# Optimization experiments

Measured on AMD Instinct MI355X. Metric: run time of the kernel, lower is better.

## Reference

```python
import jax, jax.numpy as jnp
import numpy as np

B, N, E, H = 8, 1024, 768, 8
D = E // H  # 96

def setup_inputs() -> dict:
    key = jax.random.key(0)
    ks = jax.random.split(key, 5)
    s = 0.02
    return {
        "x": jax.random.normal(ks[0], (B, N, E), dtype=jnp.float32),
        "Wqkv": jax.random.normal(ks[1], (E, 3 * E), dtype=jnp.float32) * s,
        "bqkv": jax.random.normal(ks[2], (3 * E,), dtype=jnp.float32) * s,
        "Wproj": jax.random.normal(ks[3], (E, E), dtype=jnp.float32) * s,
        "bproj": jax.random.normal(ks[4], (E,), dtype=jnp.float32) * s,
    }

def reference(x, Wqkv, bqkv, Wproj, bproj):
    # qkv: [B,N,3E] -> split as (h d qkv), qkv fastest-varying -> [B,N,H,D,3]
    qkv = (x @ Wqkv + bqkv).reshape(B, N, H, D, 3)
    q = jnp.transpose(qkv[..., 0], (0, 2, 1, 3))  # [B,H,N,D]
    k = jnp.transpose(qkv[..., 1], (0, 2, 1, 3))
    v = jnp.transpose(qkv[..., 2], (0, 2, 1, 3))
    scale = E ** (-0.5)  # note: emb_size, not head_dim (faithful to source)
    scores = jnp.einsum('bhqd,bhkd->bhqk', q, k) * scale
    attn = jax.nn.softmax(scores, axis=-1)
    out = jnp.einsum('bhqk,bhkd->bhqd', attn, v)  # [B,H,N,D]
    out = jnp.transpose(out, (0, 2, 1, 3)).reshape(B, N, E)
    return out @ Wproj + bproj
```

## Files before the change

kernel.cpp:

```cpp
#include <hip/hip_runtime.h>

typedef unsigned short u16;
typedef __attribute__((ext_vector_type(8))) short short8;
typedef __attribute__((ext_vector_type(4))) short short4v;
typedef __attribute__((ext_vector_type(4))) float f32x4;

#define DEV static __device__ __forceinline__

static_assert(sizeof(short8) == 16, "short8 must be 16B");

DEV u16 f2b(float f) {
  union { float f; unsigned u; } a; a.f = f;
  unsigned u = a.u;
  unsigned r = (u + 0x7FFFu + ((u >> 16) & 1u)) >> 16;
  return (u16)r;
}
DEV float b2f(u16 h) {
  union { unsigned u; float f; } a; a.u = ((unsigned)h) << 16;
  return a.f;
}

DEV f32x4 mfma16(short8 a, short8 b, f32x4 c) {
  asm volatile("v_mfma_f32_16x16x32_bf16 %0, %1, %2, %0" : "+v"(c) : "v"(a), "v"(b));
  return c;
}
DEV f32x4 fence_nops(f32x4 c) { asm volatile("s_nop 7\n\ts_nop 7" : "+v"(c)); return c; }
DEV f32x4 fence0(f32x4 c)     { asm volatile("" : "+v"(c)); return c; }

DEV void gl_lds16(const u16* g, u16* l) {
  __builtin_amdgcn_global_load_lds(
      (const __attribute__((address_space(1))) void*)g,
      (__attribute__((address_space(3))) void*)l, 16, 0, 0);
}

#define BAR() asm volatile("s_waitcnt lgkmcnt(0)\n\ts_barrier" ::: "memory")

constexpr int Bz = 8, Nseq = 1024, Emb = 768, Hh = 8, Dh = 96;
constexpr int Mrows = Bz * Nseq;
constexpr int K3 = 3 * Emb;
constexpr float QSCALE = 0.03608439182435161f;

__global__ __launch_bounds__(256) void k_cvt_x(const float* __restrict__ src,
                                               u16* __restrict__ dst) {
  int i = (blockIdx.x * 256 + threadIdx.x) * 4;
  float4 v = *(const float4*)(src + i);
  short4v o;
  o[0] = (short)f2b(v.x); o[1] = (short)f2b(v.y);
  o[2] = (short)f2b(v.z); o[3] = (short)f2b(v.w);
  *(short4v*)(dst + i) = o;
}

template <int PERM>
__global__ __launch_bounds__(256) void k_tcvt(const float* __restrict__ src,
                                              u16* __restrict__ dst, int R, int C) {
  __shared__ float t[32][33];
  int bx = blockIdx.x * 32;
  int by = blockIdx.y * 32;
  int c = threadIdx.x & 31, r8 = threadIdx.x >> 5;
#pragma unroll
  for (int p = 0; p < 4; ++p) {
    int r = r8 + p * 8;
    t[r][c] = src[(size_t)(by + r) * C + bx + c];
  }
  __syncthreads();
#pragma unroll
  for (int p = 0; p < 4; ++p) {
    int r = r8 + p * 8;
    int co = bx + r;
    int row = co;
    float mul = 1.f;
    if (PERM) {
      int h = co / 288, rem = co - h * 288;
      int d = rem / 3, s = rem - d * 3;
      row = s * 768 + h * 96 + d;
      if (s == 0) mul = QSCALE;
    }
    dst[(size_t)row * R + by + c] = f2b(t[c][r] * mul);
  }
}

__global__ __launch_bounds__(256) void k_permbias(const float* __restrict__ b,
                                                  float* __restrict__ bp) {
  int co = blockIdx.x * 256 + threadIdx.x;
  if (co < 2304) {
    int h = co / 288, rem = co - h * 288, d = rem / 3, s = rem - d * 3;
    bp[s * 768 + h * 96 + d] = b[co] * (s == 0 ? QSCALE : 1.f);
  }
}

template <int F32OUT>
__global__ __launch_bounds__(256, 2) void k_gemm_bt(
    const u16* __restrict__ A, const u16* __restrict__ Bt,
    const float* __restrict__ bias,
    u16* __restrict__ obf, float* __restrict__ of32,
    int Nn, int Kdim) {
  __shared__ __align__(16) u16 Al[128 * 32];
  __shared__ __align__(16) u16 Bl[128 * 32];
  int m0 = blockIdx.x * 128, n0 = blockIdx.y * 128;
  int tid = threadIdx.x;
  int w = tid >> 6, l = tid & 63, lr = l >> 4, lc = l & 15;
  int wr = w >> 1, wc = w & 1;
  f32x4 acc[4][4] = {};
  int nkt = Kdim >> 5;
  for (int kt = 0; kt < nkt; ++kt) {
    __syncthreads();
#pragma unroll
    for (int i = 0; i < 2; ++i) {
      int idx = i * 256 + tid;
      int r = idx >> 2, c8 = (idx & 3) * 8;
      gl_lds16(A + (size_t)(m0 + r) * Kdim + kt * 32 + c8, &Al[idx * 8]);
      gl_lds16(Bt + (size_t)(n0 + r) * Kdim + kt * 32 + c8, &Bl[idx * 8]);
    }
    __syncthreads();
    short8 af[4];
#pragma unroll
    for (int mi = 0; mi < 4; ++mi)
      af[mi] = *(const short8*)&Al[(wr * 64 + mi * 16 + lc) * 32 + lr * 8];
#pragma unroll
    for (int ni = 0; ni < 4; ++ni) {
      short8 bf = *(const short8*)&Bl[(wc * 64 + ni * 16 + lc) * 32 + lr * 8];
#pragma unroll
      for (int mi = 0; mi < 4; ++mi)
        acc[mi][ni] = mfma16(af[mi], bf, acc[mi][ni]);
    }
  }
  acc[3][3] = fence_nops(acc[3][3]);
#pragma unroll
  for (int mi = 0; mi < 4; ++mi)
#pragma unroll
    for (int ni = 0; ni < 4; ++ni)
      if (!(mi == 3 && ni == 3)) acc[mi][ni] = fence0(acc[mi][ni]);

#pragma unroll
  for (int mi = 0; mi < 4; ++mi) {
#pragma unroll
    for (int ni = 0; ni < 4; ++ni) {
      int col = n0 + wc * 64 + ni * 16 + lc;
      float bv = bias[col];
      int row0 = m0 + wr * 64 + mi * 16 + lr * 4;
#pragma unroll
      for (int r = 0; r < 4; ++r) {
        float v = acc[mi][ni][r] + bv;
        if (F32OUT) of32[(size_t)(row0 + r) * Nn + col] = v;
        else        obf[(size_t)(row0 + r) * Nn + col] = f2b(v);
      }
    }
  }
}

__global__ __launch_bounds__(256) void k_reshape_v(const u16* __restrict__ qkvp,
                                                   u16* __restrict__ vt) {
  __shared__ __align__(16) u16 vtile[96][136];
  int blk = blockIdx.x;
  int bh = blk >> 3, nt = blk & 7;
  int b = bh >> 3, h = bh & 7;
  int n0 = nt * 128;
  int tid = threadIdx.x;
#pragma unroll
  for (int i = 0; i < 6; ++i) {
    int task = tid + i * 256;
    int r = task / 12, g = task % 12;
    short8 vv = *(const short8*)(qkvp + (size_t)(b * 1024 + n0 + r) * 2304 +
                                 1536 + h * 96 + g * 8);
    int swz = (g & 7) << 4;
#pragma unroll
    for (int j = 0; j < 8; ++j)
      vtile[g * 8 + j][r ^ swz] = (u16)vv[j];
  }
  __syncthreads();
#pragma unroll
  for (int i = 0; i < 6; ++i) {
    int task = tid + i * 256;
    int d = task >> 4, c = task & 15;
    int swz = ((d >> 3) & 7) << 4;
    short8 v = *(const short8*)&vtile[d][(c * 8) ^ swz];
    *(short8*)(vt + ((size_t)(bh * 96) + d) * 1024 + n0 + c * 8) = v;
  }
}

__global__ __launch_bounds__(256, 2) void k_attn(const u16* __restrict__ qkvp,
                                                 const u16* __restrict__ vt,
                                                 u16* __restrict__ ctx) {
  __shared__ __align__(16) u16 reg0[17408];
  __shared__ __align__(16) u16 Vl[96 * 136];
  int blk = blockIdx.x;
  int b = blk & 7, h = (blk >> 3) & 7, qt = blk >> 6;
  int tid = threadIdx.x, w = tid >> 6, l = tid & 63;
  int lr = l >> 4, lc = l & 15;
  int q0 = qt * 128 + w * 32;
  const u16* qptr = qkvp + (size_t)b * 1024 * 2304 + h * 96;
  const u16* kptr = qptr + 768;
  const u16* vtp  = vt + (size_t)(b * 8 + h) * 96 * 1024;
  u16* Pw = reg0 + w * (32 * 136);

  short8 qf[2][3];
#pragma unroll
  for (int mf = 0; mf < 2; ++mf)
#pragma unroll
    for (int kf = 0; kf < 3; ++kf)
      qf[mf][kf] = *(const short8*)(qptr + (size_t)(q0 + mf * 16 + lc) * 2304 +
                                    kf * 32 + lr * 8);

  float mrow[2][4], lrow[2][4];
#pragma unroll
  for (int mf = 0; mf < 2; ++mf)
#pragma unroll
    for (int r = 0; r < 4; ++r) { mrow[mf][r] = -INFINITY; lrow[mf][r] = 0.f; }
  f32x4 oacc[2][6] = {};

  short8 kpre[6], vpre[6];
#pragma unroll
  for (int i = 0; i < 6; ++i) {
    int idx = tid + i * 256;
    int r = idx / 12, c = idx % 12;
    kpre[i] = *(const short8*)(kptr + (size_t)r * 2304 + c * 8);
    int d = idx >> 4, cc = idx & 15;
    vpre[i] = *(const short8*)(vtp + (size_t)d * 1024 + cc * 8);
  }

  for (int kt = 0; kt < 8; ++kt) {
    BAR();
#pragma unroll
    for (int i = 0; i < 6; ++i) {
      int idx = tid + i * 256;
      int r = idx / 12, c = idx % 12;
      *(short8*)&reg0[r * 104 + c * 8] = kpre[i];
      int d = idx >> 4, cc = idx & 15;
      *(short8*)&Vl[d * 136 + cc * 8] = vpre[i];
    }
    if (kt < 7) {
#pragma unroll
      for (int i = 0; i < 6; ++i) {
        int idx = tid + i * 256, r = idx / 12, c = idx % 12;
        kpre[i] = *(const short8*)(kptr + (size_t)((kt + 1) * 128 + r) * 2304 + c * 8);
      }
    }
    BAR();

    f32x4 sacc[2][8] = {};
#pragma unroll
    for (int nf = 0; nf < 8; ++nf) {
#pragma unroll
      for (int kf = 0; kf < 3; ++kf) {
        short8 kb = *(const short8*)&reg0[(nf * 16 + lc) * 104 + kf * 32 + lr * 8];
        sacc[0][nf] = mfma16(qf[0][kf], kb, sacc[0][nf]);
        sacc[1][nf] = mfma16(qf[1][kf], kb, sacc[1][nf]);
      }
    }
    sacc[1][7] = fence_nops(sacc[1][7]);
#pragma unroll
    for (int mf = 0; mf < 2; ++mf)
#pragma unroll
      for (int nf = 0; nf < 8; ++nf)
        if (!(mf == 1 && nf == 7)) sacc[mf][nf] = fence0(sacc[mf][nf]);

#pragma unroll
    for (int mf = 0; mf < 2; ++mf) {
#pragma unroll
      for (int r = 0; r < 4; ++r) {
        float mx = sacc[mf][0][r];
#pragma unroll
        for (int nf = 1; nf < 8; ++nf) mx = fmaxf(mx, sacc[mf][nf][r]);
#pragma unroll
        for (int d = 1; d < 16; d <<= 1) mx = fmaxf(mx, __shfl_xor(mx, d));
        float nm = fmaxf(mrow[mf][r], mx);
        float sc = __expf(mrow[mf][r] - nm);
        mrow[mf][r] = nm;
        float rs = 0.f;
#pragma unroll
        for (int nf = 0; nf < 8; ++nf) {
          float p = __expf(sacc[mf][nf][r] - nm);
          sacc[mf][nf][r] = p;
          rs += p;
        }
#pragma unroll
        for (int d = 1; d < 16; d <<= 1) rs += __shfl_xor(rs, d);
        lrow[mf][r] = lrow[mf][r] * sc + rs;
#pragma unroll
        for (int nf = 0; nf < 6; ++nf) oacc[mf][nf][r] *= sc;
      }
    }

    BAR();

#pragma unroll
    for (int mf = 0; mf < 2; ++mf)
#pragma unroll
      for (int nf = 0; nf < 8; ++nf)
#pragma unroll
        for (int r = 0; r < 4; ++r)
          Pw[(mf * 16 + lr * 4 + r) * 136 + nf * 16 + lc] = f2b(sacc[mf][nf][r]);

    if (kt < 7) {
#pragma unroll
      for (int i = 0; i < 6; ++i) {
        int idx = tid + i * 256, d = idx >> 4, cc = idx & 15;
        vpre[i] = *(const short8*)(vtp + (size_t)d * 1024 + (kt + 1) * 128 + cc * 8);
      }
    }

#pragma unroll
    for (int kf = 0; kf < 4; ++kf) {
      short8 pa0 = *(const short8*)&Pw[lc * 136 + kf * 32 + lr * 8];
      short8 pa1 = *(const short8*)&Pw[(16 + lc) * 136 + kf * 32 + lr * 8];
#pragma unroll
      for (int nf = 0; nf < 6; ++nf) {
        short8 vb = *(const short8*)&Vl[(nf * 16 + lc) * 136 + kf * 32 + lr * 8];
        oacc[0][nf] = mfma16(pa0, vb, oacc[0][nf]);
        oacc[1][nf] = mfma16(pa1, vb, oacc[1][nf]);
      }
    }
    oacc[1][5] = fence_nops(oacc[1][5]);
#pragma unroll
    for (int mf = 0; mf < 2; ++mf)
#pragma unroll
      for (int nf = 0; nf < 6; ++nf)
        if (!(mf == 1 && nf == 5)) oacc[mf][nf] = fence0(oacc[mf][nf]);
  }

#pragma unroll
  for (int mf = 0; mf < 2; ++mf) {
    float inv[4];
#pragma unroll
    for (int r = 0; r < 4; ++r) inv[r] = 1.0f / lrow[mf][r];
#pragma unroll
    for (int nf = 0; nf < 6; ++nf) {
#pragma unroll
      for (int r = 0; r < 4; ++r) {
        int row = b * 1024 + qt * 128 + w * 32 + mf * 16 + lr * 4 + r;
        ctx[(size_t)row * 768 + h * 96 + nf * 16 + lc] = f2b(oacc[mf][nf][r] * inv[r]);
      }
    }
  }
}

extern "C" void kernel_launch(void* const* d_in, const int* in_sizes, int n_in,
                              void* d_out, int out_size, void* d_ws, size_t ws_size,
                              hipStream_t stream) {
  const float* x     = (const float*)d_in[0];
  const float* Wqkv  = (const float*)d_in[1];
  const float* bqkv  = (const float*)d_in[2];
  const float* Wproj = (const float*)d_in[3];
  const float* bproj = (const float*)d_in[4];
  float* out = (float*)d_out;

  char* ws = (char*)d_ws;
  u16*   xb     = (u16*)(ws);
  u16*   wqkvT  = (u16*)(ws + 12582912);
  u16*   wprojT = (u16*)(ws + 16121856);
  float* bqkvp  = (float*)(ws + 17301504);
  u16*   qkvp   = (u16*)(ws + 17310720);
  u16*   vtb    = (u16*)(ws + 55059456);
  u16*   ctx    = xb;

  k_cvt_x<<<6144, 256, 0, stream>>>(x, xb);
  k_tcvt<1><<<dim3(K3 / 32, Emb / 32), 256, 0, stream>>>(Wqkv, wqkvT, Emb, K3);
  k_tcvt<0><<<dim3(Emb / 32, Emb / 32), 256, 0, stream>>>(Wproj, wprojT, Emb, Emb);
  k_permbias<<<9, 256, 0, stream>>>(bqkv, bqkvp);
  k_gemm_bt<0><<<dim3(Mrows / 128, K3 / 128), 256, 0, stream>>>(
      xb, wqkvT, bqkvp, qkvp, nullptr, K3, Emb);
  k_reshape_v<<<512, 256, 0, stream>>>(qkvp, vtb);
  k_attn<<<512, 256, 0, stream>>>(qkvp, vtb, ctx);
  k_gemm_bt<1><<<dim3(Mrows / 128, Emb / 128), 256, 0, stream>>>(
      ctx, wprojT, bproj, nullptr, out, Emb, Emb);
}
```

Before: 159.2 us.

## Fuse V transpose into QKV GEMM epilogue and restructure attention loop

The QKV GEMM epilogue now writes V directly in transposed layout, which removes the separate reshape kernel, and stages Q/K output tiles through LDS for coalesced 16-byte stores. The attention kernel double-buffers K tiles with direct global-to-LDS loads and reads V fragments straight from global memory instead of from LDS. It folds log2(e) into the Q scale so exp2f can be used, skips the online-softmax rescale unless the max grows past a threshold, and adds priority hints around the MFMA blocks. The epilogue writes ctx through LDS for coalesced stores. The trade-offs are more register pressure, uncached global V reads, and a lazy rescale that lets exponents grow before normalization.

```diff
diff --git a/kernel.cpp b/kernel.cpp
--- a/kernel.cpp
+++ b/kernel.cpp
@@ -15,10 +15,6 @@
   unsigned r = (u + 0x7FFFu + ((u >> 16) & 1u)) >> 16;
   return (u16)r;
 }
-DEV float b2f(u16 h) {
-  union { unsigned u; float f; } a; a.u = ((unsigned)h) << 16;
-  return a.f;
-}
 
 DEV f32x4 mfma16(short8 a, short8 b, f32x4 c) {
   asm volatile("v_mfma_f32_16x16x32_bf16 %0, %1, %2, %0" : "+v"(c) : "v"(a), "v"(b));
@@ -33,12 +29,10 @@
       (__attribute__((address_space(3))) void*)l, 16, 0, 0);
 }
 
-#define BAR() asm volatile("s_waitcnt lgkmcnt(0)\n\ts_barrier" ::: "memory")
-
 constexpr int Bz = 8, Nseq = 1024, Emb = 768, Hh = 8, Dh = 96;
 constexpr int Mrows = Bz * Nseq;
 constexpr int K3 = 3 * Emb;
-constexpr float QSCALE = 0.03608439182435161f;
+constexpr float QSCALE = 0.05205982021128899f;
 
 __global__ __launch_bounds__(256) void k_cvt_x(const float* __restrict__ src,
                                                u16* __restrict__ dst) {
@@ -88,14 +82,15 @@
   }
 }
 
-template <int F32OUT>
+template <int MODE>
 __global__ __launch_bounds__(256, 2) void k_gemm_bt(
     const u16* __restrict__ A, const u16* __restrict__ Bt,
     const float* __restrict__ bias,
-    u16* __restrict__ obf, float* __restrict__ of32,
+    u16* __restrict__ obf, u16* __restrict__ vtb, float* __restrict__ of32,
     int Nn, int Kdim) {
   __shared__ __align__(16) u16 Al[128 * 32];
   __shared__ __align__(16) u16 Bl[128 * 32];
+  __shared__ __align__(16) u16 Cst[4][32 * 88];
   int m0 = blockIdx.x * 128, n0 = blockIdx.y * 128;
   int tid = threadIdx.x;
   int w = tid >> 6, l = tid & 63, lr = l >> 4, lc = l & 15;
@@ -131,58 +126,71 @@
     for (int ni = 0; ni < 4; ++ni)
       if (!(mi == 3 && ni == 3)) acc[mi][ni] = fence0(acc[mi][ni]);
 
-#pragma unroll
-  for (int mi = 0; mi < 4; ++mi) {
-#pragma unroll
-    for (int ni = 0; ni < 4; ++ni) {
-      int col = n0 + wc * 64 + ni * 16 + lc;
-      float bv = bias[col];
-      int row0 = m0 + wr * 64 + mi * 16 + lr * 4;
-#pragma unroll
-      for (int r = 0; r < 4; ++r) {
-        float v = acc[mi][ni][r] + bv;
-        if (F32OUT) of32[(size_t)(row0 + r) * Nn + col] = v;
-        else        obf[(size_t)(row0 + r) * Nn + col] = f2b(v);
-      }
-    }
-  }
-}
-
-__global__ __launch_bounds__(256) void k_reshape_v(const u16* __restrict__ qkvp,
-                                                   u16* __restrict__ vt) {
-  __shared__ __align__(16) u16 vtile[96][136];
-  int blk = blockIdx.x;
-  int bh = blk >> 3, nt = blk & 7;
-  int b = bh >> 3, h = bh & 7;
-  int n0 = nt * 128;
-  int tid = threadIdx.x;
-#pragma unroll
-  for (int i = 0; i < 6; ++i) {
-    int task = tid + i * 256;
-    int r = task / 12, g = task % 12;
-    short8 vv = *(const short8*)(qkvp + (size_t)(b * 1024 + n0 + r) * 2304 +
-                                 1536 + h * 96 + g * 8);
-    int swz = (g & 7) << 4;
-#pragma unroll
-    for (int j = 0; j < 8; ++j)
-      vtile[g * 8 + j][r ^ swz] = (u16)vv[j];
-  }
-  __syncthreads();
-#pragma unroll
-  for (int i = 0; i < 6; ++i) {
-    int task = tid + i * 256;
-    int d = task >> 4, c = task & 15;
-    int swz = ((d >> 3) & 7) << 4;
-    short8 v = *(const short8*)&vtile[d][(c * 8) ^ swz];
-    *(short8*)(vt + ((size_t)(bh * 96) + d) * 1024 + n0 + c * 8) = v;
+  if (MODE == 0) {
+    if (n0 < 1536) {
+      u16* Cb = &Cst[w][0];
+#pragma unroll
+      for (int mi2 = 0; mi2 < 2; ++mi2) {
+#pragma unroll
+        for (int mh = 0; mh < 2; ++mh) {
+          int mi = mi2 * 2 + mh;
+#pragma unroll
+          for (int ni = 0; ni < 4; ++ni) {
+            float bv = bias[n0 + wc * 64 + ni * 16 + lc];
+#pragma unroll
+            for (int r = 0; r < 4; ++r)
+              Cb[(mh * 16 + lr * 4 + r) * 88 + ni * 16 + lc] =
+                  f2b(acc[mi][ni][r] + bv);
+          }
+        }
+#pragma unroll
+        for (int i = 0; i < 4; ++i) {
+          int idx = i * 64 + l;
+          int row = idx >> 3, c8 = idx & 7;
+          short8 vv = *(const short8*)&Cb[row * 88 + c8 * 8];
+          int grow = m0 + wr * 64 + mi2 * 32 + row;
+          int gcol = n0 + wc * 64 + c8 * 8;
+          *(short8*)(obf + (size_t)grow * Nn + gcol) = vv;
+        }
+      }
+    } else {
+#pragma unroll
+      for (int mi = 0; mi < 4; ++mi) {
+#pragma unroll
+        for (int ni = 0; ni < 4; ++ni) {
+          int col = n0 + wc * 64 + ni * 16 + lc;
+          float bv = bias[col];
+          int dall = col - 1536;
+          int row0 = m0 + wr * 64 + mi * 16 + lr * 4;
+          short4v o4;
+#pragma unroll
+          for (int r = 0; r < 4; ++r) o4[r] = (short)f2b(acc[mi][ni][r] + bv);
+          *(short4v*)(vtb + ((size_t)(row0 >> 10) * 768 + dall) * 1024 +
+                      (row0 & 1023)) = o4;
+        }
+      }
+    }
+  } else {
+#pragma unroll
+    for (int mi = 0; mi < 4; ++mi) {
+#pragma unroll
+      for (int ni = 0; ni < 4; ++ni) {
+        int col = n0 + wc * 64 + ni * 16 + lc;
+        float bv = bias[col];
+        int row0 = m0 + wr * 64 + mi * 16 + lr * 4;
+#pragma unroll
+        for (int r = 0; r < 4; ++r)
+          of32[(size_t)(row0 + r) * Nn + col] = acc[mi][ni][r] + bv;
+      }
+    }
   }
 }
 
 __global__ __launch_bounds__(256, 2) void k_attn(const u16* __restrict__ qkvp,
                                                  const u16* __restrict__ vt,
                                                  u16* __restrict__ ctx) {
-  __shared__ __align__(16) u16 reg0[17408];
-  __shared__ __align__(16) u16 Vl[96 * 136];
+  __shared__ __align__(16) u16 Kb[2][128 * 96];
+  __shared__ __align__(16) u16 Pl[4][32 * 40];
   int blk = blockIdx.x;
   int b = blk & 7, h = (blk >> 3) & 7, qt = blk >> 6;
   int tid = threadIdx.x, w = tid >> 6, l = tid & 63;
@@ -190,8 +198,16 @@
   int q0 = qt * 128 + w * 32;
   const u16* qptr = qkvp + (size_t)b * 1024 * 2304 + h * 96;
   const u16* kptr = qptr + 768;
-  const u16* vtp  = vt + (size_t)(b * 8 + h) * 96 * 1024;
-  u16* Pw = reg0 + w * (32 * 136);
+  const u16* vtp  = vt + (size_t)(b * 768 + h * 96) * 1024;
+  u16* Pw = Pl[w];
+
+  int soff[6], doff[6];
+#pragma unroll
+  for (int i = 0; i < 6; ++i) {
+    int idx = i * 256 + tid;
+    soff[i] = (idx / 12) * 2304 + (idx % 12) * 8;
+    doff[i] = idx * 8;
+  }
 
   short8 qf[2][3];
 #pragma unroll
@@ -208,45 +224,38 @@
     for (int r = 0; r < 4; ++r) { mrow[mf][r] = -INFINITY; lrow[mf][r] = 0.f; }
   f32x4 oacc[2][6] = {};
 
-  short8 kpre[6], vpre[6];
-#pragma unroll
-  for (int i = 0; i < 6; ++i) {
-    int idx = tid + i * 256;
-    int r = idx / 12, c = idx % 12;
-    kpre[i] = *(const short8*)(kptr + (size_t)r * 2304 + c * 8);
-    int d = idx >> 4, cc = idx & 15;
-    vpre[i] = *(const short8*)(vtp + (size_t)d * 1024 + cc * 8);
-  }
+#pragma unroll
+  for (int i = 0; i < 6; ++i) gl_lds16(kptr + soff[i], &Kb[0][0] + doff[i]);
+  __syncthreads();
 
   for (int kt = 0; kt < 8; ++kt) {
-    BAR();
-#pragma unroll
-    for (int i = 0; i < 6; ++i) {
-      int idx = tid + i * 256;
-      int r = idx / 12, c = idx % 12;
-      *(short8*)&reg0[r * 104 + c * 8] = kpre[i];
-      int d = idx >> 4, cc = idx & 15;
-      *(short8*)&Vl[d * 136 + cc * 8] = vpre[i];
-    }
+    const u16* Kc = Kb[kt & 1];
     if (kt < 7) {
-#pragma unroll
-      for (int i = 0; i < 6; ++i) {
-        int idx = tid + i * 256, r = idx / 12, c = idx % 12;
-        kpre[i] = *(const short8*)(kptr + (size_t)((kt + 1) * 128 + r) * 2304 + c * 8);
-      }
-    }
-    BAR();
+      const u16* kb = kptr + (size_t)(kt + 1) * 128 * 2304;
+      u16* db = Kb[(kt + 1) & 1];
+#pragma unroll
+      for (int i = 0; i < 6; ++i) gl_lds16(kb + soff[i], db + doff[i]);
+    }
 
     f32x4 sacc[2][8] = {};
+    __builtin_amdgcn_s_setprio(1);
 #pragma unroll
     for (int nf = 0; nf < 8; ++nf) {
 #pragma unroll
       for (int kf = 0; kf < 3; ++kf) {
-        short8 kb = *(const short8*)&reg0[(nf * 16 + lc) * 104 + kf * 32 + lr * 8];
+        short8 kb = *(const short8*)&Kc[(nf * 16 + lc) * 96 + kf * 32 + lr * 8];
         sacc[0][nf] = mfma16(qf[0][kf], kb, sacc[0][nf]);
         sacc[1][nf] = mfma16(qf[1][kf], kb, sacc[1][nf]);
       }
     }
+    __builtin_amdgcn_s_setprio(0);
+
+    short8 vb[2][6];
+    const u16* vkt = vtp + kt * 128;
+#pragma unroll
+    for (int nf = 0; nf < 6; ++nf)
+      vb[0][nf] = *(const short8*)(vkt + (size_t)(nf * 16 + lc) * 1024 + lr * 8);
+
     sacc[1][7] = fence_nops(sacc[1][7]);
 #pragma unroll
     for (int mf = 0; mf < 2; ++mf)
@@ -263,74 +272,84 @@
         for (int nf = 1; nf < 8; ++nf) mx = fmaxf(mx, sacc[mf][nf][r]);
 #pragma unroll
         for (int d = 1; d < 16; d <<= 1) mx = fmaxf(mx, __shfl_xor(mx, d));
-        float nm = fmaxf(mrow[mf][r], mx);
-        float sc = __expf(mrow[mf][r] - nm);
-        mrow[mf][r] = nm;
-        float rs = 0.f;
+        if (mx > mrow[mf][r] + 8.f) {
+          float sc = exp2f(mrow[mf][r] - mx);
+          mrow[mf][r] = mx;
+          lrow[mf][r] *= sc;
+#pragma unroll
+          for (int nf = 0; nf < 6; ++nf) oacc[mf][nf][r] *= sc;
+        }
+        float m = mrow[mf][r], rs = 0.f;
 #pragma unroll
         for (int nf = 0; nf < 8; ++nf) {
-          float p = __expf(sacc[mf][nf][r] - nm);
+          float p = exp2f(sacc[mf][nf][r] - m);
           sacc[mf][nf][r] = p;
           rs += p;
         }
 #pragma unroll
         for (int d = 1; d < 16; d <<= 1) rs += __shfl_xor(rs, d);
-        lrow[mf][r] = lrow[mf][r] * sc + rs;
-#pragma unroll
-        for (int nf = 0; nf < 6; ++nf) oacc[mf][nf][r] *= sc;
-      }
-    }
-
-    BAR();
-
-#pragma unroll
-    for (int mf = 0; mf < 2; ++mf)
-#pragma unroll
-      for (int nf = 0; nf < 8; ++nf)
-#pragma unroll
-        for (int r = 0; r < 4; ++r)
-          Pw[(mf * 16 + lr * 4 + r) * 136 + nf * 16 + lc] = f2b(sacc[mf][nf][r]);
-
-    if (kt < 7) {
-#pragma unroll
-      for (int i = 0; i < 6; ++i) {
-        int idx = tid + i * 256, d = idx >> 4, cc = idx & 15;
-        vpre[i] = *(const short8*)(vtp + (size_t)d * 1024 + (kt + 1) * 128 + cc * 8);
+        lrow[mf][r] += rs;
       }
     }
 
 #pragma unroll
     for (int kf = 0; kf < 4; ++kf) {
-      short8 pa0 = *(const short8*)&Pw[lc * 136 + kf * 32 + lr * 8];
-      short8 pa1 = *(const short8*)&Pw[(16 + lc) * 136 + kf * 32 + lr * 8];
+      int cb = kf & 1;
+#pragma unroll
+      for (int mf = 0; mf < 2; ++mf)
+#pragma unroll
+        for (int nn = 0; nn < 2; ++nn)
+#pragma unroll
+          for (int r = 0; r < 4; ++r)
+            Pw[(mf * 16 + lr * 4 + r) * 40 + nn * 16 + lc] =
+                f2b(sacc[mf][2 * kf + nn][r]);
+      if (kf < 3) {
+#pragma unroll
+        for (int nf = 0; nf < 6; ++nf)
+          vb[cb ^ 1][nf] = *(const short8*)(vkt + (size_t)(nf * 16 + lc) * 1024 +
+                                            (kf + 1) * 32 + lr * 8);
+      }
+      short8 pa0 = *(const short8*)&Pw[lc * 40 + lr * 8];
+      short8 pa1 = *(const short8*)&Pw[(16 + lc) * 40 + lr * 8];
+      __builtin_amdgcn_s_setprio(1);
 #pragma unroll
       for (int nf = 0; nf < 6; ++nf) {
-        short8 vb = *(const short8*)&Vl[(nf * 16 + lc) * 136 + kf * 32 + lr * 8];
-        oacc[0][nf] = mfma16(pa0, vb, oacc[0][nf]);
-        oacc[1][nf] = mfma16(pa1, vb, oacc[1][nf]);
-      }
+        oacc[0][nf] = mfma16(pa0, vb[cb][nf], oacc[0][nf]);
+        oacc[1][nf] = mfma16(pa1, vb[cb][nf], oacc[1][nf]);
+      }
+      __builtin_amdgcn_s_setprio(0);
     }
     oacc[1][5] = fence_nops(oacc[1][5]);
-#pragma unroll
-    for (int mf = 0; mf < 2; ++mf)
-#pragma unroll
-      for (int nf = 0; nf < 6; ++nf)
-        if (!(mf == 1 && nf == 5)) oacc[mf][nf] = fence0(oacc[mf][nf]);
-  }
-
-#pragma unroll
-  for (int mf = 0; mf < 2; ++mf) {
-    float inv[4];
-#pragma unroll
-    for (int r = 0; r < 4; ++r) inv[r] = 1.0f / lrow[mf][r];
-#pragma unroll
-    for (int nf = 0; nf < 6; ++nf) {
-#pragma unroll
-      for (int r = 0; r < 4; ++r) {
-        int row = b * 1024 + qt * 128 + w * 32 + mf * 16 + lr * 4 + r;
-        ctx[(size_t)row * 768 + h * 96 + nf * 16 + lc] = f2b(oacc[mf][nf][r] * inv[r]);
-      }
-    }
+
+    __syncthreads();
+  }
+
+#pragma unroll
+  for (int mf = 0; mf < 2; ++mf)
+#pragma unroll
+    for (int nf = 0; nf < 6; ++nf) oacc[mf][nf] = fence0(oacc[mf][nf]);
+
+  u16* Cw = &Kb[0][0] + w * (32 * 104);
+  float inv[2][4];
+#pragma unroll
+  for (int mf = 0; mf < 2; ++mf)
+#pragma unroll
+    for (int r = 0; r < 4; ++r) inv[mf][r] = 1.0f / lrow[mf][r];
+#pragma unroll
+  for (int mf = 0; mf < 2; ++mf)
+#pragma unroll
+    for (int nf = 0; nf < 6; ++nf)
+#pragma unroll
+      for (int r = 0; r < 4; ++r)
+        Cw[(mf * 16 + lr * 4 + r) * 104 + nf * 16 + lc] =
+            f2b(oacc[mf][nf][r] * inv[mf][r]);
+  int crow0 = b * 1024 + qt * 128 + w * 32;
+#pragma unroll
+  for (int i = 0; i < 6; ++i) {
+    int idx = i * 64 + l;
+    int row = idx / 12, c16 = idx % 12;
+    short8 vv = *(const short8*)&Cw[row * 104 + c16 * 8];
+    *(short8*)(ctx + (size_t)(crow0 + row) * 768 + h * 96 + c16 * 8) = vv;
   }
 }
 
@@ -358,9 +377,8 @@
   k_tcvt<0><<<dim3(Emb / 32, Emb / 32), 256, 0, stream>>>(Wproj, wprojT, Emb, Emb);
   k_permbias<<<9, 256, 0, stream>>>(bqkv, bqkvp);
   k_gemm_bt<0><<<dim3(Mrows / 128, K3 / 128), 256, 0, stream>>>(
-      xb, wqkvT, bqkvp, qkvp, nullptr, K3, Emb);
-  k_reshape_v<<<512, 256, 0, stream>>>(qkvp, vtb);
+      xb, wqkvT, bqkvp, qkvp, vtb, nullptr, K3, Emb);
   k_attn<<<512, 256, 0, stream>>>(qkvp, vtb, ctx);
   k_gemm_bt<1><<<dim3(Mrows / 128, Emb / 128), 256, 0, stream>>>(
-      ctx, wprojT, bproj, nullptr, out, Emb, Emb);
-}
+      ctx, wprojT, bproj, nullptr, nullptr, out, Emb, Emb);
+}
```

New measurement: 156.9 us. Within noise of the previous version (-1.4%).
